# Optimization experiments

Measured on AMD Instinct MI355X. Metric: run time of the kernel, lower is better.

## Reference

```python
import jax, jax.numpy as jnp
import numpy as np

THRESH = 64.0        # titans.surprise_threshold
NOISE_SCALE = 1e-6   # tie-breaking noise scale in _update_memory


def setup_inputs() -> dict:
    key = jax.random.key(0)
    ks = jax.random.split(key, 8)
    B, S, H, M = 2, 2048, 1024, 8192
    return {
        "hidden_states": jax.random.normal(ks[0], (B, S, H), dtype=jnp.float32),
        "memory_buffer": jax.random.normal(ks[1], (M, H), dtype=jnp.float32),
        "importance_scores": jax.random.uniform(ks[2], (M,), dtype=jnp.float32),
        "Wq": jax.random.normal(ks[3], (H, H), dtype=jnp.float32) * 0.02,
        "bq": jnp.zeros((H,), dtype=jnp.float32),
        "Wk": jax.random.normal(ks[4], (H, H), dtype=jnp.float32) * 0.02,
        "bk": jnp.zeros((H,), dtype=jnp.float32),
        "noise": jax.random.normal(ks[5], (M,), dtype=jnp.float32),
    }


def reference(hidden_states, memory_buffer, importance_scores, Wq, bq, Wk, bk, noise):
    B, S, H = hidden_states.shape
    M = memory_buffer.shape[0]

    # ---- surprise (gradient_norm method) ----
    # proxy_loss = sum((h - 0)^2)  =>  d loss / d h = 2h  =>  surprise = 2*||h||_2
    cands = hidden_states.reshape(-1, H)                      # [B*S, H]
    surprise = 2.0 * jnp.linalg.norm(cands, axis=-1)          # [B*S]

    # ---- _update_memory (torch.no_grad) ----
    # mask below-threshold candidates out, then take the (at most memory_size)
    # most surprising candidates in descending order (== argsort descending +
    # slice in the torch code; -inf entries sort last and are marked invalid).
    K = min(cands.shape[0], M)
    masked = jnp.where(surprise > THRESH, surprise, -jnp.inf)
    top_s, top_i = jax.lax.top_k(masked, K)                   # descending surprise
    valid = top_s > THRESH                                    # true only for real candidates

    # least-important memory slots (topk largest=False with tie-break noise)
    _, least_idx = jax.lax.top_k(-(importance_scores + noise * NOISE_SCALE), K)

    # scatter-write: i-th most surprising candidate -> i-th least important slot.
    # invalid lanes write to index M which is dropped (out of range).
    write_idx = jnp.where(valid, least_idx, M)                # [K]
    states_w = jax.lax.stop_gradient(cands[top_i])            # update path is no_grad
    scores_w = jax.lax.stop_gradient(jnp.where(valid, top_s, 0.0))
    new_buffer = memory_buffer.at[write_idx].set(states_w, mode="drop")   # [M, H]
    new_importance = importance_scores.at[write_idx].set(scores_w, mode="drop")
    del new_importance  # bookkeeping state; does not affect retrieved output

    # ---- query (cross-attention over memory) ----
    q = hidden_states @ Wq.T + bq                             # [B, S, H]
    mk = new_buffer @ Wk.T + bk                               # [M, H]
    scores = jnp.einsum("bsh,mh->bsm", q, mk) * (H ** -0.5)
    attn = jax.nn.softmax(scores, axis=-1)                    # [B, S, M]
    retrieved = jnp.einsum("bsm,mh->bsh", attn, new_buffer)   # [B, S, H]
    return retrieved
```

## Files before the change

kernel.cpp:

```cpp
#include <hip/hip_runtime.h>
#include <hip/hip_bf16.h>
#include <math.h>
#include <stdint.h>

typedef __attribute__((ext_vector_type(4))) float floatx4;
typedef __attribute__((ext_vector_type(8))) short shortx8;
typedef __attribute__((ext_vector_type(4))) unsigned short ushortx4;

#define BS_CAND 4096
#define HDIM    1024
#define MSLOTS  8192
#define THRESH  64.0f
#define PV_SPLIT 4
#define PS_COLS 128

__device__ __forceinline__ unsigned short f2b_bits(float f) {
    __hip_bfloat16 b = __float2bfloat16(f);
    return *(unsigned short*)&b;
}
__device__ __forceinline__ float b2f_bits(unsigned short u) {
    return __uint_as_float(((unsigned)u) << 16);
}

__device__ __forceinline__ float blockReduceSum(float x) {
    __shared__ float red[4];
    #pragma unroll
    for (int o = 32; o > 0; o >>= 1) x += __shfl_down(x, o, 64);
    int lane = threadIdx.x & 63, w = threadIdx.x >> 6;
    if (lane == 0) red[w] = x;
    __syncthreads();
    float s = red[0] + red[1] + red[2] + red[3];
    __syncthreads();
    return s;
}

__global__ __launch_bounds__(256) void pre_k(const float* __restrict__ h,
                                             float* __restrict__ sur,
                                             __hip_bfloat16* __restrict__ Hbf,
                                             const float* __restrict__ imp,
                                             const float* __restrict__ noi,
                                             float* __restrict__ keys,
                                             int* __restrict__ row_src,
                                             const float* __restrict__ Wq,
                                             __hip_bfloat16* __restrict__ Wqbf,
                                             const float* __restrict__ Wk,
                                             __hip_bfloat16* __restrict__ Wkbf) {
    int b = blockIdx.x;
    if (b < BS_CAND) {
        float4 v = ((const float4*)(h + (size_t)b * HDIM))[threadIdx.x];
        ushortx4 o;
        o.x = f2b_bits(v.x); o.y = f2b_bits(v.y);
        o.z = f2b_bits(v.z); o.w = f2b_bits(v.w);
        ((ushortx4*)(Hbf + (size_t)b * HDIM))[threadIdx.x] = o;
        float s = v.x * v.x + v.y * v.y + v.z * v.z + v.w * v.w;
        float tot = blockReduceSum(s);
        if (threadIdx.x == 0) sur[b] = 2.0f * sqrtf(tot);
    } else if (b < BS_CAND + MSLOTS / 256) {
        int i = (b - BS_CAND) * 256 + threadIdx.x;
        keys[i] = imp[i] + noi[i] * 1e-6f;
        row_src[i] = -1;
    } else {
        int w = b - (BS_CAND + MSLOTS / 256);
        const float* in = (w < 1024) ? Wq : Wk;
        __hip_bfloat16* out = (w < 1024) ? Wqbf : Wkbf;
        int j = (w & 1023) * 256 + threadIdx.x;
        float4 v = ((const float4*)in)[j];
        ushortx4 o;
        o.x = f2b_bits(v.x); o.y = f2b_bits(v.y);
        o.z = f2b_bits(v.z); o.w = f2b_bits(v.w);
        ((ushortx4*)out)[j] = o;
    }
}

__global__ __launch_bounds__(256) void ranks_k(const float* __restrict__ sur,
                                               int* __restrict__ cand_ord,
                                               const float* __restrict__ keys,
                                               int* __restrict__ slot_ord) {
    int b = blockIdx.x;
    if (b < BS_CAND) {
        float ki = sur[b];
        float cnt = 0.f;
        for (int j = threadIdx.x; j < BS_CAND; j += 256) {
            float kj = sur[j];
            cnt += ((kj > ki) || (kj == ki && j < b)) ? 1.f : 0.f;
        }
        float r = blockReduceSum(cnt);
        if (threadIdx.x == 0) cand_ord[(int)r] = b;
    } else {
        int i = b - BS_CAND;
        float ki = keys[i];
        float cnt = 0.f;
        for (int j = threadIdx.x; j < MSLOTS; j += 256) {
            float kj = keys[j];
            cnt += ((kj < ki) || (kj == ki && j < i)) ? 1.f : 0.f;
        }
        float r = blockReduceSum(cnt);
        if (threadIdx.x == 0) slot_ord[(int)r] = i;
    }
}

__global__ __launch_bounds__(256) void scatter_k(const int* __restrict__ cand_order,
                                                 const int* __restrict__ slot_order,
                                                 const float* __restrict__ sur,
                                                 int* __restrict__ row_src) {
    int i = blockIdx.x * 256 + threadIdx.x;
    int c = cand_order[i];
    if (sur[c] > THRESH) row_src[slot_order[i]] = c;
}

__global__ __launch_bounds__(256) void build_b_k(const float* __restrict__ mem,
                                                 const float* __restrict__ hid,
                                                 const int* __restrict__ src,
                                                 __hip_bfloat16* __restrict__ B) {
    int m = blockIdx.x;
    int s = src[m];
    const float4* r = (const float4*)((s < 0) ? (mem + (size_t)m * HDIM)
                                              : (hid + (size_t)s * HDIM));
    float4 v = r[threadIdx.x];
    ushortx4 o;
    o.x = f2b_bits(v.x); o.y = f2b_bits(v.y);
    o.z = f2b_bits(v.z); o.w = f2b_bits(v.w);
    ((ushortx4*)(B + (size_t)m * HDIM))[threadIdx.x] = o;
}

__global__ __launch_bounds__(256) void transpose_k(const __hip_bfloat16* __restrict__ in,
                                                   __hip_bfloat16* __restrict__ out,
                                                   int R, int C) {
    __shared__ __hip_bfloat16 t[64][65];
    int cb = blockIdx.x * 64, rb = blockIdx.y * 64;
    int tx = threadIdx.x & 63, ty = threadIdx.x >> 6;
    #pragma unroll
    for (int k = 0; k < 16; k++) {
        int r = ty * 16 + k;
        t[r][tx] = in[(size_t)(rb + r) * C + cb + tx];
    }
    __syncthreads();
    #pragma unroll
    for (int k = 0; k < 16; k++) {
        int c = ty * 16 + k;
        out[(size_t)(cb + c) * R + rb + tx] = t[tx][c];
    }
}

__device__ __forceinline__ void load_lds16(const __hip_bfloat16* g, __hip_bfloat16* l) {
    __builtin_amdgcn_global_load_lds(
        (const __attribute__((address_space(1))) void*)g,
        (__attribute__((address_space(3))) void*)l, 16, 0, 0);
}

template <int EPI, int SWAP>
__global__ __launch_bounds__(512, 2) void gemm_bt(const __hip_bfloat16* __restrict__ A,
                                                  const __hip_bfloat16* __restrict__ Bt,
                                                  const __hip_bfloat16* __restrict__ Bt2,
                                                  __hip_bfloat16* __restrict__ outH,
                                                  const float* __restrict__ bias,
                                                  const float* __restrict__ bias2,
                                                  float* __restrict__ ps,
                                                  int rows0b,
                                                  int M, int N, int K, int ksplit,
                                                  float scale) {
    extern __shared__ char lds[];
    const int tid = threadIdx.x;
    const int wave = tid >> 6, lane = tid & 63;
    const int lm = lane & 15, lq = lane >> 4;
    const int wm = wave >> 2, wn = wave & 3;
    const int bm = SWAP ? blockIdx.x : blockIdx.y;
    const int bn = SWAP ? blockIdx.y : blockIdx.x;
    const int kb = blockIdx.z * ksplit;
    const int niters = ksplit >> 7;

    const __hip_bfloat16* BtSel = (EPI == 1 && bm >= rows0b) ? Bt2 : Bt;
    const float* biasSel = (EPI == 1 && bm >= rows0b) ? bias2 : bias;

    const int l8 = lane >> 3;
    const int colsrc = ((((lane & 7) << 4) ^ (l8 << 4)) >> 1);
    const __hip_bfloat16* Abase = A + (size_t)bm * 256 * K;
    const __hip_bfloat16* Bbase = BtSel + (size_t)bn * 256 * K;
    const __hip_bfloat16* srcA[2][2];
    const __hip_bfloat16* srcB[2][2];
    #pragma unroll
    for (int h = 0; h < 2; h++)
        #pragma unroll
        for (int t = 0; t < 2; t++) {
            int row = t * 128 + h * 64 + wave * 8 + l8;
            srcA[h][t] = Abase + (size_t)row * K + colsrc;
            srcB[h][t] = Bbase + (size_t)row * K + colsrc;
        }

    const int cxor = (lq << 4) ^ ((lm & 7) << 4);
    const int a_b0 = (wm * 64 + lm) * 128 + cxor;
    const int a_b1 = a_b0 ^ 64;
    const int b_b0 = (wn * 32 + lm) * 128 + cxor;
    const int b_b1 = b_b0 ^ 64;

    floatx4 acc[8][4];
    #pragma unroll
    for (int i = 0; i < 8; i++)
        #pragma unroll
        for (int j = 0; j < 4; j++) acc[i][j] = {0.f, 0.f, 0.f, 0.f};

    shortx8 af[4][2], bf[2][2];

#define LDSV(off) (*(const shortx8*)(lds + (off)))
#define READ_A(g, bo) do {                                                  \
    const int ab_ = (bo) + (g) * 16384;                                     \
    af[0][0] = LDSV(ab_ + a_b0);        af[0][1] = LDSV(ab_ + a_b1);        \
    af[1][0] = LDSV(ab_ + a_b0 + 2048); af[1][1] = LDSV(ab_ + a_b1 + 2048); \
    af[2][0] = LDSV(ab_ + a_b0 + 4096); af[2][1] = LDSV(ab_ + a_b1 + 4096); \
    af[3][0] = LDSV(ab_ + a_b0 + 6144); af[3][1] = LDSV(ab_ + a_b1 + 6144); \
} while (0)
#define READ_B(g, bo) do {                                                  \
    const int bb_ = (bo) + 32768 + (g) * 16384;                             \
    bf[0][0] = LDSV(bb_ + b_b0);        bf[0][1] = LDSV(bb_ + b_b1);        \
    bf[1][0] = LDSV(bb_ + b_b0 + 2048); bf[1][1] = LDSV(bb_ + b_b1 + 2048); \
} while (0)
#define STAGE(xs, h, buf, kofs) do {                                        \
    char* d_ = lds + (buf) * 65536 + (xs) * 32768 + (h) * 16384 + wave * 1024; \
    load_lds16(((xs) ? srcB : srcA)[h][0] + (kofs), (__hip_bfloat16*)d_);   \
    load_lds16(((xs) ? srcB : srcA)[h][1] + (kofs), (__hip_bfloat16*)(d_ + 8192)); \
} while (0)
#define MFQ(mh, nh) do {                                                    \
    __builtin_amdgcn_s_setprio(1);                                          \
    _Pragma("unroll")                                                       \
    for (int ii_ = 0; ii_ < 4; ii_++)                                       \
        _Pragma("unroll")                                                   \
        for (int jj_ = 0; jj_ < 2; jj_++) {                                 \
            acc[(mh)*4+ii_][(nh)*2+jj_] = __builtin_amdgcn_mfma_f32_16x16x32_bf16( \
                af[ii_][0], bf[jj_][0], acc[(mh)*4+ii_][(nh)*2+jj_], 0, 0, 0); \
            acc[(mh)*4+ii_][(nh)*2+jj_] = __builtin_amdgcn_mfma_f32_16x16x32_bf16( \
                af[ii_][1], bf[jj_][1], acc[(mh)*4+ii_][(nh)*2+jj_], 0, 0, 0); \
        }                                                                   \
    __builtin_amdgcn_s_setprio(0);                                          \
} while (0)
#define BAR() __builtin_amdgcn_s_barrier()
#define LGKM0() asm volatile("s_waitcnt lgkmcnt(0)" ::: "memory")
#define VMC6() asm volatile("s_waitcnt vmcnt(6)" ::: "memory")
#define VMC0() asm volatile("s_waitcnt vmcnt(0)" ::: "memory")

    STAGE(0, 0, 0, kb);
    STAGE(1, 1, 0, kb);
    STAGE(0, 1, 0, kb);
    STAGE(1, 0, 0, kb);
    STAGE(0, 0, 1, kb + 64);
    STAGE(1, 1, 1, kb + 64);
    STAGE(0, 1, 1, kb + 64);
    VMC6();
    BAR();

#define ITER(E, kcur, knext) do {                                           \
                                         \
    READ_A(0, 0); READ_B(0, 0); STAGE(1, 0, 1, (kcur) + 64);                \
    BAR(); LGKM0(); MFQ(0, 0); BAR();                                       \
                                                                   \
    READ_B(1, 0); if (E) STAGE(0, 0, 0, (knext));                           \
    BAR(); LGKM0(); MFQ(0, 1); BAR();                                       \
                                                                   \
    READ_A(1, 0); if (E) STAGE(1, 1, 0, (knext));                           \
    BAR(); LGKM0(); MFQ(1, 1); BAR();                                       \
                                                                   \
    READ_B(0, 0);                                                           \
    if (E) { STAGE(0, 1, 0, (knext)); VMC6(); } else { VMC0(); }            \
    BAR(); LGKM0(); MFQ(1, 0); BAR();                                       \
                                         \
    READ_A(0, 65536); READ_B(0, 65536); if (E) STAGE(1, 0, 0, (knext));     \
    BAR(); LGKM0(); MFQ(0, 0); BAR();                                       \
                                                                   \
    READ_B(1, 65536); if (E) STAGE(0, 0, 1, (knext) + 64);                  \
    BAR(); LGKM0(); MFQ(0, 1); BAR();                                       \
                                                                   \
    READ_A(1, 65536); if (E) STAGE(1, 1, 1, (knext) + 64);                  \
    BAR(); LGKM0(); MFQ(1, 1); BAR();                                       \
                                                                   \
    READ_B(0, 65536); if (E) { STAGE(0, 1, 1, (knext) + 64); VMC6(); }      \
    BAR(); LGKM0(); MFQ(1, 0); BAR();                                       \
} while (0)

    int it = 0;
    #pragma unroll 1
    for (; it < niters - 1; ++it) {
        const int kc = kb + it * 128;
        ITER(1, kc, kc + 128);
    }
    {
        const int kc = kb + it * 128;
        ITER(0, kc, 0);
    }

#undef ITER
#undef LDSV
#undef READ_A
#undef READ_B
#undef STAGE
#undef MFQ
#undef BAR
#undef LGKM0
#undef VMC6
#undef VMC0

    if (EPI == 2) {
        #pragma unroll
        for (int i = 0; i < 8; i++) {
            const int grow0 = bm * 256 + wm * 128 + (i >> 2) * 64 + (i & 3) * 16 + lq * 4;
            #pragma unroll
            for (int r = 0; r < 4; r++) {
                float rs = 0.f;
                #pragma unroll
                for (int j = 0; j < 4; j++) {
                    const int gcol = bn * 256 + (wn >> 1) * 128 + (j >> 1) * 64 +
                                     (wn & 1) * 32 + (j & 1) * 16 + lm;
                    float e = __expf(acc[i][j][r] * scale);
                    unsigned short eb = f2b_bits(e);
                    ((unsigned short*)outH)[(size_t)(grow0 + r) * N + gcol] = eb;
                    rs += b2f_bits(eb);
                }
                rs += __shfl_xor(rs, 1, 64);
                rs += __shfl_xor(rs, 2, 64);
                rs += __shfl_xor(rs, 4, 64);
                rs += __shfl_xor(rs, 8, 64);
                if (lm == 0)
                    ps[(size_t)(grow0 + r) * PS_COLS + bn * 4 + wn] = rs;
            }
        }
    } else {
        __hip_bfloat16* outHz = outH + ((EPI == 4) ? (size_t)blockIdx.z * M * N : 0);
        #pragma unroll
        for (int i = 0; i < 8; i++) {
            const int grow0 = bm * 256 + wm * 128 + (i >> 2) * 64 + (i & 3) * 16 + lq * 4;
            #pragma unroll
            for (int j = 0; j < 4; j++) {
                const int gcol = bn * 256 + (wn >> 1) * 128 + (j >> 1) * 64 +
                                 (wn & 1) * 32 + (j & 1) * 16 + lm;
                #pragma unroll
                for (int r = 0; r < 4; r++) {
                    float v = acc[i][j][r];
                    size_t idx = (size_t)(grow0 + r) * N + gcol;
                    if (EPI == 1) outHz[idx] = __float2bfloat16(v + biasSel[gcol]);
                    else          outHz[idx] = __float2bfloat16(v * scale);
                }
            }
        }
    }
}

__global__ __launch_bounds__(256) void reduce4_k(const ushortx4* __restrict__ part,
                                                 const float* __restrict__ ps,
                                                 float4* __restrict__ out) {
    int row = blockIdx.x;
    float s = 0.f;
    if (threadIdx.x < PS_COLS) s = ps[(size_t)row * PS_COLS + threadIdx.x];
    float tot = blockReduceSum(s);
    float inv = 1.f / tot;
    size_t base = (size_t)row * (HDIM / 4) + threadIdx.x;
    const size_t stride = (size_t)BS_CAND * (HDIM / 4);
    float4 o = {0.f, 0.f, 0.f, 0.f};
    #pragma unroll
    for (int z = 0; z < PV_SPLIT; z++) {
        ushortx4 p = part[base + (size_t)z * stride];
        o.x += b2f_bits(p.x); o.y += b2f_bits(p.y);
        o.z += b2f_bits(p.z); o.w += b2f_bits(p.w);
    }
    o.x *= inv; o.y *= inv; o.z *= inv; o.w *= inv;
    out[(size_t)row * (HDIM / 4) + threadIdx.x] = o;
}

extern "C" void kernel_launch(void* const* d_in, const int* in_sizes, int n_in,
                              void* d_out, int out_size, void* d_ws, size_t ws_size,
                              hipStream_t stream) {
    const float* hidden = (const float*)d_in[0];
    const float* membuf = (const float*)d_in[1];
    const float* imp    = (const float*)d_in[2];
    const float* Wq     = (const float*)d_in[3];
    const float* bq     = (const float*)d_in[4];
    const float* Wk     = (const float*)d_in[5];
    const float* bk     = (const float*)d_in[6];
    const float* noise  = (const float*)d_in[7];

    static bool s_attr = false;
    if (!s_attr) {
        (void)hipFuncSetAttribute((const void*)gemm_bt<1, 0>,
                                  hipFuncAttributeMaxDynamicSharedMemorySize, 131072);
        (void)hipFuncSetAttribute((const void*)gemm_bt<2, 0>,
                                  hipFuncAttributeMaxDynamicSharedMemorySize, 131072);
        (void)hipFuncSetAttribute((const void*)gemm_bt<4, 1>,
                                  hipFuncAttributeMaxDynamicSharedMemorySize, 131072);
        s_attr = true;
    }

    char* ws = (char*)d_ws;
    size_t off = 0;
    auto alloc = [&](size_t bytes) -> void* {
        void* p = ws + off;
        off += (bytes + 255) & ~(size_t)255;
        return p;
    };
    float*          surprise = (float*)alloc(BS_CAND * 4);
    float*          skeys    = (float*)alloc(MSLOTS * 4);
    float*          ps       = (float*)alloc((size_t)BS_CAND * PS_COLS * 4);
    int*            cand_ord = (int*)alloc(BS_CAND * 4);
    int*            slot_ord = (int*)alloc(MSLOTS * 4);
    int*            row_src  = (int*)alloc(MSLOTS * 4);
    __hip_bfloat16* Wqbf = (__hip_bfloat16*)alloc((size_t)HDIM * HDIM * 2);
    __hip_bfloat16* Wkbf = (__hip_bfloat16*)alloc((size_t)HDIM * HDIM * 2);
    __hip_bfloat16* BbfT = (__hip_bfloat16*)alloc((size_t)HDIM * MSLOTS * 2);
    size_t s_base = off;
    __hip_bfloat16* Sbf = (__hip_bfloat16*)(ws + s_base);
    __hip_bfloat16* Hbf = (__hip_bfloat16*)(ws + s_base);
    __hip_bfloat16* Bbf = (__hip_bfloat16*)(ws + s_base + (size_t)BS_CAND * HDIM * 2);
    off = s_base + ((size_t)BS_CAND * MSLOTS * 2 + 255) & ~(size_t)255;
    size_t t_base = off;
    __hip_bfloat16* qbf  = (__hip_bfloat16*)alloc((size_t)BS_CAND * HDIM * 2);
    __hip_bfloat16* mkbf = (__hip_bfloat16*)alloc((size_t)MSLOTS * HDIM * 2);
    __hip_bfloat16* part = (__hip_bfloat16*)(ws + t_base);

    pre_k<<<BS_CAND + MSLOTS / 256 + 2048, 256, 0, stream>>>(
        hidden, surprise, Hbf, imp, noise, skeys, row_src, Wq, Wqbf, Wk, Wkbf);
    ranks_k<<<BS_CAND + MSLOTS, 256, 0, stream>>>(surprise, cand_ord, skeys, slot_ord);
    scatter_k<<<BS_CAND / 256, 256, 0, stream>>>(cand_ord, slot_ord, surprise, row_src);
    build_b_k<<<MSLOTS, 256, 0, stream>>>(membuf, hidden, row_src, Bbf);
    transpose_k<<<dim3(HDIM / 64, MSLOTS / 64), 256, 0, stream>>>(Bbf, BbfT, MSLOTS, HDIM);
    gemm_bt<1, 0><<<dim3(HDIM / 256, (BS_CAND + MSLOTS) / 256), 512, 131072, stream>>>(
        Hbf, Wqbf, Wkbf, qbf, bq, bk, nullptr, BS_CAND / 256,
        BS_CAND + MSLOTS, HDIM, HDIM, HDIM, 1.f);
    gemm_bt<2, 0><<<dim3(MSLOTS / 256, BS_CAND / 256), 512, 131072, stream>>>(
        qbf, mkbf, nullptr, Sbf, nullptr, nullptr, ps, 1 << 30,
        BS_CAND, MSLOTS, HDIM, HDIM, 0.03125f);
    gemm_bt<4, 1><<<dim3(BS_CAND / 256, HDIM / 256, PV_SPLIT), 512, 131072, stream>>>(
        Sbf, BbfT, nullptr, part, nullptr, nullptr, nullptr, 1 << 30,
        BS_CAND, HDIM, MSLOTS, MSLOTS / PV_SPLIT, 1.f);
    reduce4_k<<<BS_CAND, 256, 0, stream>>>((const ushortx4*)part, ps, (float4*)d_out);
}
```

Measured before the change: 316.0 us.

## Stage GEMM epilogue through swizzled LDS for coalesced 16-byte global stores

The epilogue now writes the bf16 output tile into LDS with an XOR swizzle, synchronises, then has each thread write 16-byte vectors of contiguous row segments to global memory. This replaces the scattered 2-byte stores per lane. It also adds partial lgkmcnt(8) waits before some barriers in the main loop to drain LDS reads earlier. The cost is an extra LDS round trip and a block-wide barrier in the epilogue, and it assumes a 512-thread block and a 256x256 tile.

```diff
diff --git a/kernel.cpp b/kernel.cpp
--- a/kernel.cpp
+++ b/kernel.cpp
@@ -234,6 +234,7 @@
 } while (0)
 #define BAR() __builtin_amdgcn_s_barrier()
 #define LGKM0() asm volatile("s_waitcnt lgkmcnt(0)" ::: "memory")
+#define LGKM8() asm volatile("s_waitcnt lgkmcnt(8)" ::: "memory")
 #define VMC6() asm volatile("s_waitcnt vmcnt(6)" ::: "memory")
 #define VMC0() asm volatile("s_waitcnt vmcnt(0)" ::: "memory")
 
@@ -248,8 +249,8 @@
     BAR();
 
 #define ITER(E, kcur, knext) do {                                           \
-                                         \
-    READ_A(0, 0); READ_B(0, 0); STAGE(1, 0, 1, (kcur) + 64);                \
+                                                                   \
+    READ_A(0, 0); READ_B(0, 0); STAGE(1, 0, 1, (kcur) + 64); LGKM8();       \
     BAR(); LGKM0(); MFQ(0, 0); BAR();                                       \
                                                                    \
     READ_B(1, 0); if (E) STAGE(0, 0, 0, (knext));                           \
@@ -261,8 +262,9 @@
     READ_B(0, 0);                                                           \
     if (E) { STAGE(0, 1, 0, (knext)); VMC6(); } else { VMC0(); }            \
     BAR(); LGKM0(); MFQ(1, 0); BAR();                                       \
-                                         \
+                                                                   \
     READ_A(0, 65536); READ_B(0, 65536); if (E) STAGE(1, 0, 0, (knext));     \
+    LGKM8();                                                                \
     BAR(); LGKM0(); MFQ(0, 0); BAR();                                       \
                                                                    \
     READ_B(1, 65536); if (E) STAGE(0, 0, 1, (knext) + 64);                  \
@@ -294,23 +296,27 @@
 #undef MFQ
 #undef BAR
 #undef LGKM0
+#undef LGKM8
 #undef VMC6
 #undef VMC0
 
+    unsigned short* scr = (unsigned short*)lds;
     if (EPI == 2) {
         #pragma unroll
         for (int i = 0; i < 8; i++) {
-            const int grow0 = bm * 256 + wm * 128 + (i >> 2) * 64 + (i & 3) * 16 + lq * 4;
+            const int ribase = wm * 128 + (i >> 2) * 64 + (i & 3) * 16 + lq * 4;
             #pragma unroll
             for (int r = 0; r < 4; r++) {
+                const int ri = ribase + r;
+                const int xr = ((lq * 4 + r) & 7) << 3;
                 float rs = 0.f;
                 #pragma unroll
                 for (int j = 0; j < 4; j++) {
-                    const int gcol = bn * 256 + (wn >> 1) * 128 + (j >> 1) * 64 +
-                                     (wn & 1) * 32 + (j & 1) * 16 + lm;
+                    const int c = (wn >> 1) * 128 + (j >> 1) * 64 +
+                                  (wn & 1) * 32 + (j & 1) * 16 + lm;
                     float e = __expf(acc[i][j][r] * scale);
                     unsigned short eb = f2b_bits(e);
-                    ((unsigned short*)outH)[(size_t)(grow0 + r) * N + gcol] = eb;
+                    scr[ri * 256 + (c ^ xr)] = eb;
                     rs += b2f_bits(eb);
                 }
                 rs += __shfl_xor(rs, 1, 64);
@@ -318,26 +324,39 @@
                 rs += __shfl_xor(rs, 4, 64);
                 rs += __shfl_xor(rs, 8, 64);
                 if (lm == 0)
-                    ps[(size_t)(grow0 + r) * PS_COLS + bn * 4 + wn] = rs;
+                    ps[(size_t)(bm * 256 + ri) * PS_COLS + bn * 4 + wn] = rs;
             }
         }
     } else {
+        #pragma unroll
+        for (int i = 0; i < 8; i++) {
+            const int ribase = wm * 128 + (i >> 2) * 64 + (i & 3) * 16 + lq * 4;
+            #pragma unroll
+            for (int j = 0; j < 4; j++) {
+                const int c = (wn >> 1) * 128 + (j >> 1) * 64 +
+                              (wn & 1) * 32 + (j & 1) * 16 + lm;
+                const float badd = (EPI == 1) ? biasSel[bn * 256 + c] : 0.f;
+                #pragma unroll
+                for (int r = 0; r < 4; r++) {
+                    const int ri = ribase + r;
+                    const int xr = ((lq * 4 + r) & 7) << 3;
+                    float v = acc[i][j][r];
+                    float o = (EPI == 1) ? (v + badd) : (v * scale);
+                    scr[ri * 256 + (c ^ xr)] = f2b_bits(o);
+                }
+            }
+        }
+    }
+    __syncthreads();
+    {
         __hip_bfloat16* outHz = outH + ((EPI == 4) ? (size_t)blockIdx.z * M * N : 0);
         #pragma unroll
-        for (int i = 0; i < 8; i++) {
-            const int grow0 = bm * 256 + wm * 128 + (i >> 2) * 64 + (i & 3) * 16 + lq * 4;
-            #pragma unroll
-            for (int j = 0; j < 4; j++) {
-                const int gcol = bn * 256 + (wn >> 1) * 128 + (j >> 1) * 64 +
-                                 (wn & 1) * 32 + (j & 1) * 16 + lm;
-                #pragma unroll
-                for (int r = 0; r < 4; r++) {
-                    float v = acc[i][j][r];
-                    size_t idx = (size_t)(grow0 + r) * N + gcol;
-                    if (EPI == 1) outHz[idx] = __float2bfloat16(v + biasSel[gcol]);
-                    else          outHz[idx] = __float2bfloat16(v * scale);
-                }
-            }
+        for (int p = 0; p < 16; p++) {
+            const int t = p * 512 + tid;
+            const int ri = t >> 5, ch = t & 31;
+            const int c8 = ch * 8;
+            shortx8 v = *(const shortx8*)(scr + ri * 256 + (c8 ^ ((ri & 7) << 3)));
+            *(shortx8*)(outHz + (size_t)(bm * 256 + ri) * N + bn * 256 + c8) = v;
         }
     }
 }
```

New measurement: 322.8 us. 1.02x slower.

## Fuse buffer build with transpose and keep both B-fragment halves in registers

Applied to the files above, without the earlier changes.

Merges the kernel that gathers memory/hidden rows into a bf16 buffer with the transpose kernel, so each tile is converted once and written both row-major and transposed without re-reading the intermediate. In the GEMM main loop, the two B-fragment halves are held in separate register sets so the redundant LDS re-reads of B before the final quadrant are removed. This trades extra VGPR pressure for fewer LDS reads, and the fused kernel now does scalar 2-byte global loads and stores instead of vectorized float4 ones.

```diff
diff --git a/kernel.cpp b/kernel.cpp
--- a/kernel.cpp
+++ b/kernel.cpp
@@ -108,37 +108,29 @@
     if (sur[c] > THRESH) row_src[slot_order[i]] = c;
 }
 
-__global__ __launch_bounds__(256) void build_b_k(const float* __restrict__ mem,
-                                                 const float* __restrict__ hid,
-                                                 const int* __restrict__ src,
-                                                 __hip_bfloat16* __restrict__ B) {
-    int m = blockIdx.x;
-    int s = src[m];
-    const float4* r = (const float4*)((s < 0) ? (mem + (size_t)m * HDIM)
-                                              : (hid + (size_t)s * HDIM));
-    float4 v = r[threadIdx.x];
-    ushortx4 o;
-    o.x = f2b_bits(v.x); o.y = f2b_bits(v.y);
-    o.z = f2b_bits(v.z); o.w = f2b_bits(v.w);
-    ((ushortx4*)(B + (size_t)m * HDIM))[threadIdx.x] = o;
-}
-
-__global__ __launch_bounds__(256) void transpose_k(const __hip_bfloat16* __restrict__ in,
-                                                   __hip_bfloat16* __restrict__ out,
-                                                   int R, int C) {
-    __shared__ __hip_bfloat16 t[64][65];
+__global__ __launch_bounds__(256) void bbt_k(const float* __restrict__ mem,
+                                             const float* __restrict__ hid,
+                                             const int* __restrict__ src,
+                                             __hip_bfloat16* __restrict__ B,
+                                             __hip_bfloat16* __restrict__ BT) {
+    __shared__ unsigned short t[64][72];
     int cb = blockIdx.x * 64, rb = blockIdx.y * 64;
     int tx = threadIdx.x & 63, ty = threadIdx.x >> 6;
     #pragma unroll
     for (int k = 0; k < 16; k++) {
         int r = ty * 16 + k;
-        t[r][tx] = in[(size_t)(rb + r) * C + cb + tx];
+        int s = src[rb + r];
+        const float* row = (s < 0) ? (mem + (size_t)(rb + r) * HDIM)
+                                   : (hid + (size_t)s * HDIM);
+        unsigned short b = f2b_bits(row[cb + tx]);
+        t[r][tx] = b;
+        ((unsigned short*)B)[(size_t)(rb + r) * HDIM + cb + tx] = b;
     }
     __syncthreads();
     #pragma unroll
     for (int k = 0; k < 16; k++) {
         int c = ty * 16 + k;
-        out[(size_t)(cb + c) * R + rb + tx] = t[tx][c];
+        ((unsigned short*)BT)[(size_t)(cb + c) * MSLOTS + rb + tx] = t[tx][c];
     }
 }
 
@@ -199,7 +191,7 @@
         #pragma unroll
         for (int j = 0; j < 4; j++) acc[i][j] = {0.f, 0.f, 0.f, 0.f};
 
-    shortx8 af[4][2], bf[2][2];
+    shortx8 af[4][2], bf0h[2][2], bf1h[2][2];
 
 #define LDSV(off) (*(const shortx8*)(lds + (off)))
 #define READ_A(g, bo) do {                                                  \
@@ -209,26 +201,26 @@
     af[2][0] = LDSV(ab_ + a_b0 + 4096); af[2][1] = LDSV(ab_ + a_b1 + 4096); \
     af[3][0] = LDSV(ab_ + a_b0 + 6144); af[3][1] = LDSV(ab_ + a_b1 + 6144); \
 } while (0)
-#define READ_B(g, bo) do {                                                  \
+#define READ_B(dst, g, bo) do {                                             \
     const int bb_ = (bo) + 32768 + (g) * 16384;                             \
-    bf[0][0] = LDSV(bb_ + b_b0);        bf[0][1] = LDSV(bb_ + b_b1);        \
-    bf[1][0] = LDSV(bb_ + b_b0 + 2048); bf[1][1] = LDSV(bb_ + b_b1 + 2048); \
+    dst[0][0] = LDSV(bb_ + b_b0);        dst[0][1] = LDSV(bb_ + b_b1);      \
+    dst[1][0] = LDSV(bb_ + b_b0 + 2048); dst[1][1] = LDSV(bb_ + b_b1 + 2048);\
 } while (0)
 #define STAGE(xs, h, buf, kofs) do {                                        \
     char* d_ = lds + (buf) * 65536 + (xs) * 32768 + (h) * 16384 + wave * 1024; \
     load_lds16(((xs) ? srcB : srcA)[h][0] + (kofs), (__hip_bfloat16*)d_);   \
     load_lds16(((xs) ? srcB : srcA)[h][1] + (kofs), (__hip_bfloat16*)(d_ + 8192)); \
 } while (0)
-#define MFQ(mh, nh) do {                                                    \
+#define MFQ(mh, nh, BF) do {                                                \
     __builtin_amdgcn_s_setprio(1);                                          \
     _Pragma("unroll")                                                       \
     for (int ii_ = 0; ii_ < 4; ii_++)                                       \
         _Pragma("unroll")                                                   \
         for (int jj_ = 0; jj_ < 2; jj_++) {                                 \
             acc[(mh)*4+ii_][(nh)*2+jj_] = __builtin_amdgcn_mfma_f32_16x16x32_bf16( \
-                af[ii_][0], bf[jj_][0], acc[(mh)*4+ii_][(nh)*2+jj_], 0, 0, 0); \
+                af[ii_][0], BF[jj_][0], acc[(mh)*4+ii_][(nh)*2+jj_], 0, 0, 0); \
             acc[(mh)*4+ii_][(nh)*2+jj_] = __builtin_amdgcn_mfma_f32_16x16x32_bf16( \
-                af[ii_][1], bf[jj_][1], acc[(mh)*4+ii_][(nh)*2+jj_], 0, 0, 0); \
+                af[ii_][1], BF[jj_][1], acc[(mh)*4+ii_][(nh)*2+jj_], 0, 0, 0); \
         }                                                                   \
     __builtin_amdgcn_s_setprio(0);                                          \
 } while (0)
@@ -248,31 +240,30 @@
     BAR();
 
 #define ITER(E, kcur, knext) do {                                           \
-                                         \
-    READ_A(0, 0); READ_B(0, 0); STAGE(1, 0, 1, (kcur) + 64);                \
-    BAR(); LGKM0(); MFQ(0, 0); BAR();                                       \
-                                                                   \
-    READ_B(1, 0); if (E) STAGE(0, 0, 0, (knext));                           \
-    BAR(); LGKM0(); MFQ(0, 1); BAR();                                       \
+                                                                   \
+    READ_A(0, 0); READ_B(bf0h, 0, 0); STAGE(1, 0, 1, (kcur) + 64);          \
+    BAR(); LGKM0(); MFQ(0, 0, bf0h); BAR();                                 \
+                                                                   \
+    READ_B(bf1h, 1, 0); if (E) STAGE(0, 0, 0, (knext));                     \
+    BAR(); LGKM0(); MFQ(0, 1, bf1h); BAR();                                 \
                                                                    \
     READ_A(1, 0); if (E) STAGE(1, 1, 0, (knext));                           \
-    BAR(); LGKM0(); MFQ(1, 1); BAR();                                       \
-                                                                   \
-    READ_B(0, 0);                                                           \
+    BAR(); LGKM0(); MFQ(1, 1, bf1h); BAR();                                 \
+                                     \
     if (E) { STAGE(0, 1, 0, (knext)); VMC6(); } else { VMC0(); }            \
-    BAR(); LGKM0(); MFQ(1, 0); BAR();                                       \
-                                         \
-    READ_A(0, 65536); READ_B(0, 65536); if (E) STAGE(1, 0, 0, (knext));     \
-    BAR(); LGKM0(); MFQ(0, 0); BAR();                                       \
-                                                                   \
-    READ_B(1, 65536); if (E) STAGE(0, 0, 1, (knext) + 64);                  \
-    BAR(); LGKM0(); MFQ(0, 1); BAR();                                       \
+    BAR(); LGKM0(); MFQ(1, 0, bf0h); BAR();                                 \
+                                                                   \
+    READ_A(0, 65536); READ_B(bf0h, 0, 65536); if (E) STAGE(1, 0, 0, (knext)); \
+    BAR(); LGKM0(); MFQ(0, 0, bf0h); BAR();                                 \
+                                                                   \
+    READ_B(bf1h, 1, 65536); if (E) STAGE(0, 0, 1, (knext) + 64);            \
+    BAR(); LGKM0(); MFQ(0, 1, bf1h); BAR();                                 \
                                                                    \
     READ_A(1, 65536); if (E) STAGE(1, 1, 1, (knext) + 64);                  \
-    BAR(); LGKM0(); MFQ(1, 1); BAR();                                       \
-                                                                   \
-    READ_B(0, 65536); if (E) { STAGE(0, 1, 1, (knext) + 64); VMC6(); }      \
-    BAR(); LGKM0(); MFQ(1, 0); BAR();                                       \
+    BAR(); LGKM0(); MFQ(1, 1, bf1h); BAR();                                 \
+                                                         \
+    if (E) { STAGE(0, 1, 1, (knext) + 64); VMC6(); }                        \
+    BAR(); LGKM0(); MFQ(1, 0, bf0h); BAR();                                 \
 } while (0)
 
     int it = 0;
@@ -416,8 +407,8 @@
         hidden, surprise, Hbf, imp, noise, skeys, row_src, Wq, Wqbf, Wk, Wkbf);
     ranks_k<<<BS_CAND + MSLOTS, 256, 0, stream>>>(surprise, cand_ord, skeys, slot_ord);
     scatter_k<<<BS_CAND / 256, 256, 0, stream>>>(cand_ord, slot_ord, surprise, row_src);
-    build_b_k<<<MSLOTS, 256, 0, stream>>>(membuf, hidden, row_src, Bbf);
-    transpose_k<<<dim3(HDIM / 64, MSLOTS / 64), 256, 0, stream>>>(Bbf, BbfT, MSLOTS, HDIM);
+    bbt_k<<<dim3(HDIM / 64, MSLOTS / 64), 256, 0, stream>>>(
+        membuf, hidden, row_src, Bbf, BbfT);
     gemm_bt<1, 0><<<dim3(HDIM / 256, (BS_CAND + MSLOTS) / 256), 512, 131072, stream>>>(
         Hbf, Wqbf, Wkbf, qbf, bq, bk, nullptr, BS_CAND / 256,
         BS_CAND + MSLOTS, HDIM, HDIM, HDIM, 1.f);
```

Result: no change. 312.5 us (-1.1%).
